# Performance work log

Measured on AMD Instinct MI355X. Metric: run time of the kernel, lower is better.

Reference implementation:

```python
import jax, jax.numpy as jnp
import numpy as np

B, S, D = 1, 2048, 2048
H, G, HD = 32, 8, 64
EPS = 1e-6
ROPE_BASE = 10000.0


def rms_norm(x, g):
    # torch RMSNorm computed in fp32 then cast back (PytorchRMSNorm wrapper)
    xf = x.astype(jnp.float32)
    y = xf * jax.lax.rsqrt(jnp.mean(xf * xf, axis=-1, keepdims=True) + EPS) * g.astype(jnp.float32)
    return y.astype(x.dtype)


def rotate_half(x):
    x1, x2 = jnp.split(x, 2, axis=-1)
    return jnp.concatenate([-x2, x1], axis=-1)


def apply_rope(x, cos, sin):
    # x: (b, h, s, hd); cos/sin: (s, hd)
    return x * cos[None, None] + rotate_half(x) * sin[None, None]


def setup_inputs() -> dict:
    key = jax.random.key(0)
    ks = jax.random.split(key, 8)
    x = jax.random.normal(ks[0], (B, S, D), dtype=jnp.float32)
    wq = jax.random.normal(ks[1], (H * HD, D), dtype=jnp.float32) * (D ** -0.5)
    wk = jax.random.normal(ks[2], (G * HD, D), dtype=jnp.float32) * (D ** -0.5)
    wv = jax.random.normal(ks[3], (G * HD, D), dtype=jnp.float32) * (D ** -0.5)
    wo = jax.random.normal(ks[4], (D, H * HD), dtype=jnp.float32) * (D ** -0.5)
    qg = jnp.ones((HD,), dtype=jnp.float32)
    kg = jnp.ones((HD,), dtype=jnp.float32)
    # RoPE tables (HF-style: duplicated half-dim frequencies)
    inv_freq = 1.0 / (ROPE_BASE ** (jnp.arange(0, HD, 2, dtype=jnp.float32) / HD))
    ang = jnp.arange(S, dtype=jnp.float32)[:, None] * inv_freq[None, :]  # (S, HD/2)
    emb = jnp.concatenate([ang, ang], axis=-1)  # (S, HD)
    cos = jnp.cos(emb)
    sin = jnp.sin(emb)
    # causal mask: True = future (upper-right triangle)
    mask = jnp.triu(jnp.ones((S, S), dtype=bool), k=1)
    return {"x": x, "mask": mask, "cos": cos, "sin": sin,
            "wq": wq, "wk": wk, "wv": wv, "wo": wo, "qg": qg, "kg": kg}


def reference(x, mask, cos, sin, wq, wk, wv, wo, qg, kg):
    b, s, _ = x.shape
    rep = H // G
    q = (x @ wq.T).reshape(b, s, H, HD).transpose(0, 2, 1, 3)   # (b,H,s,hd)
    k = (x @ wk.T).reshape(b, s, G, HD).transpose(0, 2, 1, 3)   # (b,G,s,hd)
    v = (x @ wv.T).reshape(b, s, G, HD).transpose(0, 2, 1, 3)
    q = rms_norm(q, qg)
    k = rms_norm(k, kg)
    q = apply_rope(q, cos[:s], sin[:s])
    k = apply_rope(k, cos[:s], sin[:s])
    k = jnp.repeat(k, rep, axis=1)  # (b,H,s,hd) GQA expansion
    v = jnp.repeat(v, rep, axis=1)
    scores = jnp.einsum('bhqd,bhkd->bhqk', q, k) * (HD ** -0.5)
    neg = jnp.finfo(scores.dtype).min / 2
    scores = jnp.where(mask[None, None, :s, :s], neg, scores)
    w = jax.nn.softmax(scores, axis=-1)
    ctx = jnp.einsum('bhqk,bhkd->bhqd', w, v)
    ctx = ctx.transpose(0, 2, 1, 3).reshape(b, s, H * HD)
    return ctx @ wo.T
```

## Files before the change

kernel.cpp:

```cpp
#include <hip/hip_runtime.h>
#include <stdint.h>

#define SEQ    2048
#define DMODEL 2048
#define NHEAD  32
#define NKV    8
#define HDIM   64
#define NQKV   3072

typedef __bf16 bf16x8 __attribute__((ext_vector_type(8)));
typedef float  f32x4  __attribute__((ext_vector_type(4)));

#define SCALE2 0.180336880f
#define THR2   12.0f

__device__ __forceinline__ ushort bf(float f){
  __bf16 h = (__bf16)f;
  return __builtin_bit_cast(unsigned short, h);
}
__device__ __forceinline__ float b2f(ushort v){
  union { uint32_t u; float f; } a; a.u = ((uint32_t)v) << 16; return a.f;
}
__device__ __forceinline__ float ex2(float x){
  return __builtin_amdgcn_exp2f(x);
}
__device__ __forceinline__ float fmax3(float a, float b, float c){
  float r;
  asm("v_max3_f32 %0, %1, %2, %3" : "=v"(r) : "v"(a), "v"(b), "v"(c));
  return r;
}

__device__ __forceinline__ void gl_lds16(const void* g, void* l){
  __builtin_amdgcn_global_load_lds(
      (const __attribute__((address_space(1))) uint32_t*)g,
      (__attribute__((address_space(3))) uint32_t*)l, 16, 0, 0);
}

__global__ __launch_bounds__(256) void k_cvt_all(const float* __restrict__ x,
                                                 const float* __restrict__ wq,
                                                 const float* __restrict__ wk,
                                                 const float* __restrict__ wv,
                                                 const float* __restrict__ wo,
                                                 ushort* __restrict__ xb,
                                                 ushort* __restrict__ wcat,
                                                 ushort* __restrict__ wob){
  int i = blockIdx.x * 256 + threadIdx.x;
  const float* src; ushort* dst; int s4; int d4;
  if (i < 1048576)      { src = x;  dst = xb;   s4 = i;           d4 = s4; }
  else if (i < 2097152) { src = wq; dst = wcat; s4 = i - 1048576; d4 = s4; }
  else if (i < 2359296) { src = wk; dst = wcat; s4 = i - 2097152; d4 = s4 + 1048576; }
  else if (i < 2621440) { src = wv; dst = wcat; s4 = i - 2359296; d4 = s4 + 1310720; }
  else                  { src = wo; dst = wob;  s4 = i - 2621440; d4 = s4; }
  float4 v = reinterpret_cast<const float4*>(src)[s4];
  ushort4 o;
  o.x = bf(v.x); o.y = bf(v.y); o.z = bf(v.z); o.w = bf(v.w);
  reinterpret_cast<ushort4*>(dst)[d4] = o;
}

__global__ __launch_bounds__(256) void k_gemm_bt(const ushort* __restrict__ A,
                                                 const ushort* __restrict__ B,
                                                 float* __restrict__ C,
                                                 int M, int N, int K){
  __shared__ ushort As[2][128*64];
  __shared__ ushort Bs[2][64*64];
  const int tid = threadIdx.x, lane = tid & 63, wid = tid >> 6;
  const int bm = blockIdx.y * 128, bn = blockIdx.x * 64;
  const int wr = wid >> 1, wc = wid & 1;
  const int l15 = lane & 15, u = lane >> 4;

  const int crow = lane >> 3;
  const int scol = ((lane & 7) ^ crow) * 8;
  const ushort* Abase = A + (size_t)(bm + wid*32 + crow) * K + scol;
  const ushort* Bbase = B + (size_t)(bn + wid*16 + crow) * K + scol;

  auto STAGE = [&](int buf, int k0){
#pragma unroll
    for (int c = 0; c < 4; c++)
      gl_lds16(Abase + k0 + (size_t)c*8*K, &As[buf][(wid*32 + c*8)*64]);
#pragma unroll
    for (int c = 0; c < 2; c++)
      gl_lds16(Bbase + k0 + (size_t)c*8*K, &Bs[buf][(wid*16 + c*8)*64]);
  };

  f32x4 acc[4][2] = {};
  const int NT = K >> 6;

  STAGE(0, 0);
  __syncthreads();

  for (int t = 0; t < NT; t++){
    const int cur = t & 1;
    if (t + 1 < NT) STAGE(cur ^ 1, (t + 1) << 6);

#pragma unroll
    for (int kc = 0; kc < 2; kc++){
      bf16x8 af[4], bfr[2];
#pragma unroll
      for (int m = 0; m < 4; m++){
        int row = wr*64 + m*16 + l15;
        af[m] = *reinterpret_cast<const bf16x8*>(&As[cur][row*64 + (((kc*4+u) ^ (row&7))*8)]);
      }
#pragma unroll
      for (int n = 0; n < 2; n++){
        int row = wc*32 + n*16 + l15;
        bfr[n] = *reinterpret_cast<const bf16x8*>(&Bs[cur][row*64 + (((kc*4+u) ^ (row&7))*8)]);
      }
      __builtin_amdgcn_s_setprio(1);
#pragma unroll
      for (int m = 0; m < 4; m++)
#pragma unroll
        for (int n = 0; n < 2; n++)
          acc[m][n] = __builtin_amdgcn_mfma_f32_16x16x32_bf16(af[m], bfr[n], acc[m][n], 0, 0, 0);
      __builtin_amdgcn_s_setprio(0);
    }

    __syncthreads();
  }

#pragma unroll
  for (int m = 0; m < 4; m++)
#pragma unroll
    for (int n = 0; n < 2; n++)
#pragma unroll
      for (int j = 0; j < 4; j++){
        int row = bm + wr*64 + m*16 + u*4 + j;
        int col = bn + wc*32 + n*16 + l15;
        C[(size_t)row * N + col] = acc[m][n][j];
      }
}

__global__ __launch_bounds__(256) void k_gemm_btc(const ushort* __restrict__ A,
                                                  const ushort* __restrict__ B,
                                                  ushort* __restrict__ C,
                                                  int M, int N, int K){
  __shared__ ushort As[2][128*64];
  __shared__ ushort Bs[2][96*64];
  const int tid = threadIdx.x, lane = tid & 63, wid = tid >> 6;
  const int bm = blockIdx.y * 128, bn = blockIdx.x * 96;
  const int wr = wid >> 1, wc = wid & 1;
  const int l15 = lane & 15, u = lane >> 4;

  const int crow = lane >> 3;
  const int scol = ((lane & 7) ^ crow) * 8;
  const ushort* Abase = A + (size_t)(bm + wid*32 + crow) * K + scol;
  const ushort* Bbase = B + (size_t)(bn + wid*24 + crow) * K + scol;

  auto STAGE = [&](int buf, int k0){
#pragma unroll
    for (int c = 0; c < 4; c++)
      gl_lds16(Abase + k0 + (size_t)c*8*K, &As[buf][(wid*32 + c*8)*64]);
#pragma unroll
    for (int c = 0; c < 3; c++)
      gl_lds16(Bbase + k0 + (size_t)c*8*K, &Bs[buf][(wid*24 + c*8)*64]);
  };

  f32x4 acc[4][3] = {};
  const int NT = K >> 6;

  STAGE(0, 0);
  __syncthreads();

  for (int t = 0; t < NT; t++){
    const int cur = t & 1;
    if (t + 1 < NT) STAGE(cur ^ 1, (t + 1) << 6);

#pragma unroll
    for (int kc = 0; kc < 2; kc++){
      bf16x8 af[4], bfr[3];
#pragma unroll
      for (int m = 0; m < 4; m++){
        int row = wr*64 + m*16 + l15;
        af[m] = *reinterpret_cast<const bf16x8*>(&As[cur][row*64 + (((kc*4+u) ^ (row&7))*8)]);
      }
#pragma unroll
      for (int n = 0; n < 3; n++){
        int row = wc*48 + n*16 + l15;
        bfr[n] = *reinterpret_cast<const bf16x8*>(&Bs[cur][row*64 + (((kc*4+u) ^ (row&7))*8)]);
      }
      __builtin_amdgcn_s_setprio(1);
#pragma unroll
      for (int m = 0; m < 4; m++)
#pragma unroll
        for (int n = 0; n < 3; n++)
          acc[m][n] = __builtin_amdgcn_mfma_f32_16x16x32_bf16(af[m], bfr[n], acc[m][n], 0, 0, 0);
      __builtin_amdgcn_s_setprio(0);
    }

    __syncthreads();
  }

#pragma unroll
  for (int m = 0; m < 4; m++)
#pragma unroll
    for (int n = 0; n < 3; n++)
#pragma unroll
      for (int j = 0; j < 4; j++){
        int row = bm + wr*64 + m*16 + u*4 + j;
        int col = bn + wc*48 + n*16 + l15;
        C[(size_t)row * N + col] = bf(acc[m][n][j]);
      }
}

__global__ __launch_bounds__(256) void k_normrope(const ushort* __restrict__ qkvc,
                                                  const float* __restrict__ cosp,
                                                  const float* __restrict__ sinp,
                                                  const float* __restrict__ qg,
                                                  const float* __restrict__ kg,
                                                  ushort* __restrict__ qb,
                                                  ushort* __restrict__ kb){
  const int s = blockIdx.x;
  const int tid = threadIdx.x, lane = tid & 63, wid = tid >> 6;
  const ushort* row = qkvc + (size_t)s * NQKV;
  const float cs = cosp[s*HDIM + lane];
  const float sn = sinp[s*HDIM + lane];

  for (int hidx = wid; hidx < 40; hidx += 4){
    const bool isq = hidx < 32;
    const int col = isq ? hidx*64 : 2048 + (hidx-32)*64;
    float x = b2f(row[col + lane]);
    float ss = x * x;
#pragma unroll
    for (int m = 1; m < 64; m <<= 1) ss += __shfl_xor(ss, m);
    float r = rsqrtf(ss * (1.0f/64.0f) + 1e-6f);
    float y = x * r * (isq ? qg : kg)[lane];
    float p = __shfl_xor(y, 32);
    float out = y * cs + (lane < 32 ? -p : p) * sn;
    if (isq) qb[(size_t)s*2048 + hidx*64 + lane] = bf(out * SCALE2);
    else     kb[(size_t)s*512 + (hidx-32)*64 + lane] = bf(out);
  }
}

__global__ __launch_bounds__(256) void k_vtrans(const ushort* __restrict__ qkvc,
                                                ushort* __restrict__ vtb){
  __shared__ ushort tile[64][68];
  const int g = blockIdx.x >> 5, st = blockIdx.x & 31;
  const int tid = threadIdx.x;
#pragma unroll
  for (int i = 0; i < 4; i++){
    int idx = i*256 + tid;
    int r = idx >> 4, c4 = idx & 15;
    ushort4 v = *reinterpret_cast<const ushort4*>(
        qkvc + (size_t)(st*64 + r)*NQKV + 2560 + g*64 + c4*4);
    tile[c4*4+0][r] = v.x;
    tile[c4*4+1][r] = v.y;
    tile[c4*4+2][r] = v.z;
    tile[c4*4+3][r] = v.w;
  }
  __syncthreads();
#pragma unroll
  for (int i = 0; i < 4; i++){
    int idx = i*256 + tid;
    int d = idx >> 4, s4 = idx & 15;
    int pos4 = (s4 >> 3)*32 + (s4 & 3)*8 + ((s4 >> 2) & 1)*4;
    ushort4 o = *reinterpret_cast<const ushort4*>(&tile[d][s4*4]);
    *reinterpret_cast<ushort4*>(vtb + (size_t)(g*64 + d)*SEQ + st*64 + pos4) = o;
  }
}

__global__ __launch_bounds__(256) void k_attn(const ushort* __restrict__ qbuf,
                                              const ushort* __restrict__ kbuf,
                                              const ushort* __restrict__ vtb,
                                              ushort* __restrict__ op,
                                              float2* __restrict__ ml){
  __shared__ ushort Kd[2][64*64];
  __shared__ ushort Vd[2][64*64];

  const int bx = blockIdx.x;
  const int qt   = 31 - (bx >> 6);
  const int part = (bx >> 5) & 1;
  const int h    = bx & 31;
  const int g = h >> 2;
  const int n  = qt + 1;
  const int h1 = (n + 1) >> 1;
  const int t0 = part ? h1 : 0;
  const int t1 = part ? n  : h1;
  const int tid = threadIdx.x, lane = tid & 63, wid = tid >> 6;
  const int l15 = lane & 15, u = lane >> 4;
  const int q0 = qt*64 + wid*16;

  bf16x8 qf[2];
#pragma unroll
  for (int kc = 0; kc < 2; kc++)
    qf[kc] = *reinterpret_cast<const bf16x8*>(
        qbuf + (size_t)(q0 + l15)*2048 + h*64 + kc*32 + u*8);

  f32x4 o[4] = {};
  float mrun = -1e30f;
  float lrun = 0.f;

  int koff[8], voff[8];
#pragma unroll
  for (int kb = 0; kb < 4; kb++)
#pragma unroll
    for (int kc = 0; kc < 2; kc++){
      int keyl = kb*16 + l15;
      koff[kb*2+kc] = (keyl*64 + (((kc*4+u) ^ (keyl&7))*8)) * 2;
    }
#pragma unroll
  for (int kc = 0; kc < 2; kc++)
#pragma unroll
    for (int d0 = 0; d0 < 4; d0++){
      int vrow = d0*16 + l15;
      voff[kc*4+d0] = (vrow*64 + (((kc*4+u) ^ (vrow&7))*8)) * 2;
    }

  const int srow = wid*16 + (lane >> 3);
  const int scol = ((lane & 7) ^ (lane >> 3)) * 8;
  const ushort* ksrc0 = kbuf + (size_t)srow*512 + g*64 + scol;
  const ushort* vsrc0 = vtb  + (size_t)(g*64 + srow)*SEQ + scol;

  auto STAGE = [&](int buf, int t){
    const ushort* ks = ksrc0 + (size_t)t*64*512;
    gl_lds16(ks,         &Kd[buf][wid*1024]);
    gl_lds16(ks + 8*512, &Kd[buf][wid*1024 + 512]);
    const ushort* vs = vsrc0 + t*64;
    gl_lds16(vs,          &Vd[buf][wid*1024]);
    gl_lds16(vs + 8*SEQ,  &Vd[buf][wid*1024 + 512]);
  };

  if (t0 < t1){
    STAGE(0, t0);
    __syncthreads();

    for (int t = t0; t < t1; t++){
      const int cur = (t - t0) & 1;
      if (t + 1 < t1) STAGE(cur ^ 1, t + 1);

      const char* KB = (const char*)Kd + cur*8192;
      const char* VB = (const char*)Vd + cur*8192;
      const bool full = (t*64 + 63) <= q0;

      f32x4 st[4];
#pragma unroll
      for (int kb = 0; kb < 4; kb++){
        const int key0 = t*64 + kb*16;
        if (key0 <= q0 + 15){
          bf16x8 kf0 = *reinterpret_cast<const bf16x8*>(KB + koff[kb*2]);
          bf16x8 kf1 = *reinterpret_cast<const bf16x8*>(KB + koff[kb*2+1]);
          f32x4 a = {};
          a = __builtin_amdgcn_mfma_f32_16x16x32_bf16(kf0, qf[0], a, 0, 0, 0);
          a = __builtin_amdgcn_mfma_f32_16x16x32_bf16(kf1, qf[1], a, 0, 0, 0);
          st[kb] = a;
        } else {
          st[kb] = (f32x4){-1e30f, -1e30f, -1e30f, -1e30f};
        }
      }
      if (!full){
        const int keyb = t*64 + u*4;
        const int qr = q0 + l15;
#pragma unroll
        for (int kb = 0; kb < 4; kb++)
#pragma unroll
          for (int j = 0; j < 4; j++)
            st[kb][j] = (keyb + kb*16 + j > qr) ? -1e30f : st[kb][j];
      }

      {
        float r0 = fmax3(st[0][0], st[0][1], st[0][2]);
        float r1 = fmax3(st[0][3], st[1][0], st[1][1]);
        float r2 = fmax3(st[1][2], st[1][3], st[2][0]);
        float r3 = fmax3(st[2][1], st[2][2], st[2][3]);
        float r4 = fmax3(st[3][0], st[3][1], st[3][2]);
        float m0 = fmax3(r0, r1, r2);
        float m1 = fmax3(r3, r4, st[3][3]);
        float tml = fmaxf(m0, m1);
        if (__any(tml > mrun + THR2)){
          float tm = fmaxf(tml, __shfl_xor(tml, 16));
          tm = fmaxf(tm, __shfl_xor(tm, 32));
          float mn = fmaxf(mrun, tm);
          float al = ex2(mrun - mn);
          mrun = mn;
          lrun *= al;
#pragma unroll
          for (int d0 = 0; d0 < 4; d0++)
#pragma unroll
            for (int j = 0; j < 4; j++) o[d0][j] *= al;
        }
        float ls[4];
#pragma unroll
        for (int kb = 0; kb < 4; kb++){
          float p0 = ex2(st[kb][0] - mrun);
          float p1 = ex2(st[kb][1] - mrun);
          float p2 = ex2(st[kb][2] - mrun);
          float p3 = ex2(st[kb][3] - mrun);
          st[kb][0] = p0; st[kb][1] = p1; st[kb][2] = p2; st[kb][3] = p3;
          ls[kb] = (p0 + p1) + (p2 + p3);
        }
        lrun += (ls[0] + ls[1]) + (ls[2] + ls[3]);
      }

      __builtin_amdgcn_s_setprio(1);
#pragma unroll
      for (int kc = 0; kc < 2; kc++){
        union { uint32_t w[4]; bf16x8 v; } pb;
        asm("v_cvt_pk_bf16_f32 %0, %1, %2" : "=v"(pb.w[0]) : "v"(st[2*kc  ][0]), "v"(st[2*kc  ][1]));
        asm("v_cvt_pk_bf16_f32 %0, %1, %2" : "=v"(pb.w[1]) : "v"(st[2*kc  ][2]), "v"(st[2*kc  ][3]));
        asm("v_cvt_pk_bf16_f32 %0, %1, %2" : "=v"(pb.w[2]) : "v"(st[2*kc+1][0]), "v"(st[2*kc+1][1]));
        asm("v_cvt_pk_bf16_f32 %0, %1, %2" : "=v"(pb.w[3]) : "v"(st[2*kc+1][2]), "v"(st[2*kc+1][3]));
#pragma unroll
        for (int d0 = 0; d0 < 4; d0++){
          bf16x8 vb8 = *reinterpret_cast<const bf16x8*>(VB + voff[kc*4+d0]);
          o[d0] = __builtin_amdgcn_mfma_f32_16x16x32_bf16(vb8, pb.v, o[d0], 0, 0, 0);
        }
      }
      __builtin_amdgcn_s_setprio(0);

      __syncthreads();
    }
  }

  {
    float lt = lrun + __shfl_xor(lrun, 16);
    lt += __shfl_xor(lt, 32);
    float inv = lt > 0.f ? 1.0f / lt : 0.f;
    const size_t ridx = (size_t)part*65536 + h*2048 + (q0 + l15);
#pragma unroll
    for (int d0 = 0; d0 < 4; d0++){
      ushort4 w;
      w.x = bf(o[d0][0] * inv); w.y = bf(o[d0][1] * inv);
      w.z = bf(o[d0][2] * inv); w.w = bf(o[d0][3] * inv);
      *reinterpret_cast<ushort4*>(&op[ridx*64 + d0*16 + u*4]) = w;
    }
    if (lane < 16) ml[ridx] = make_float2(mrun, lt);
  }
}

__global__ __launch_bounds__(256) void k_comb(const ushort* __restrict__ op,
                                              const float2* __restrict__ ml,
                                              ushort* __restrict__ ctx){
  const int tq = blockIdx.x*256 + threadIdx.x;
  const int q = tq & 3, row = (tq >> 2) & 2047, h = tq >> 13;
  const int idx = h*2048 + row;
  float2 a = ml[idx], b = ml[idx + 65536];
  float m = fmaxf(a.x, b.x);
  float w0 = ex2(a.x - m) * a.y;
  float w1 = ex2(b.x - m) * b.y;
  float inv = 1.0f / (w0 + w1);
  w0 *= inv; w1 *= inv;
  const ushort4* p0 = reinterpret_cast<const ushort4*>(op + (size_t)idx*64 + q*16);
  const ushort4* p1 = reinterpret_cast<const ushort4*>(op + ((size_t)idx + 65536)*64 + q*16);
  ushort* dst = ctx + (size_t)row*2048 + h*64 + q*16;
#pragma unroll
  for (int i = 0; i < 4; i++){
    ushort4 x0 = p0[i], x1 = p1[i];
    ushort4 w;
    w.x = bf(w0*b2f(x0.x) + w1*b2f(x1.x));
    w.y = bf(w0*b2f(x0.y) + w1*b2f(x1.y));
    w.z = bf(w0*b2f(x0.z) + w1*b2f(x1.z));
    w.w = bf(w0*b2f(x0.w) + w1*b2f(x1.w));
    reinterpret_cast<ushort4*>(dst)[i] = w;
  }
}

extern "C" void kernel_launch(void* const* d_in, const int* in_sizes, int n_in,
                              void* d_out, int out_size, void* d_ws, size_t ws_size,
                              hipStream_t stream){
  const float* x    = (const float*)d_in[0];
  const float* cosp = (const float*)d_in[2];
  const float* sinp = (const float*)d_in[3];
  const float* wq   = (const float*)d_in[4];
  const float* wk   = (const float*)d_in[5];
  const float* wv   = (const float*)d_in[6];
  const float* wo   = (const float*)d_in[7];
  const float* qg   = (const float*)d_in[8];
  const float* kg   = (const float*)d_in[9];
  float* out = (float*)d_out;

  char* ws = (char*)d_ws;
  ushort* xb   = (ushort*)(ws);
  ushort* wcat = (ushort*)(ws + 8388608);
  ushort* wob  = (ushort*)(ws + 20971520);
  ushort* qkvc = (ushort*)(ws + 29360128);
  ushort* qb   = (ushort*)(ws + 41943040);
  ushort* kb   = (ushort*)(ws + 50331648);
  ushort* vtb  = (ushort*)(ws + 52428800);
  ushort* ctxb = (ushort*)(ws + 54525952);
  ushort* op   = (ushort*)(ws);
  float2* ml   = (float2*)(ws + 16777216);

  k_cvt_all<<<14336, 256, 0, stream>>>(x, wq, wk, wv, wo, xb, wcat, wob);
  k_gemm_btc<<<dim3(32, 16), 256, 0, stream>>>(xb, wcat, qkvc, 2048, 3072, 2048);
  k_normrope<<<2048, 256, 0, stream>>>(qkvc, cosp, sinp, qg, kg, qb, kb);
  k_vtrans<<<256, 256, 0, stream>>>(qkvc, vtb);
  k_attn<<<2048, 256, 0, stream>>>(qb, kb, vtb, op, ml);
  k_comb<<<1024, 256, 0, stream>>>(op, ml, ctxb);
  k_gemm_bt<<<dim3(32, 16), 256, 0, stream>>>(ctxb, wob, out, 2048, 2048, 2048);
}
```

Measured before the change: 135.6 us.

## Process 128-row query tiles per block to reuse K/V fragments across two sub-tiles

Each wave now handles 32 query rows (two 16-row sub-tiles) instead of 16, so every K and V fragment read from LDS feeds two MFMAs. The grid is halved and the split-KV scheme is rewritten so each 128-row tile splits its causal key range evenly into two parts. Query tiles are paired (j and 15-j) to balance the causal work across blocks. This doubles accumulator and score registers per thread, and the kernel now asks for 4 blocks per CU via launch bounds, which risks register spills.

```diff
diff --git a/kernel.cpp b/kernel.cpp
--- a/kernel.cpp
+++ b/kernel.cpp
@@ -257,36 +257,37 @@
   }
 }
 
-__global__ __launch_bounds__(256) void k_attn(const ushort* __restrict__ qbuf,
-                                              const ushort* __restrict__ kbuf,
-                                              const ushort* __restrict__ vtb,
-                                              ushort* __restrict__ op,
-                                              float2* __restrict__ ml){
+__global__ __launch_bounds__(256, 4) void k_attn(const ushort* __restrict__ qbuf,
+                                                 const ushort* __restrict__ kbuf,
+                                                 const ushort* __restrict__ vtb,
+                                                 ushort* __restrict__ op,
+                                                 float2* __restrict__ ml){
   __shared__ ushort Kd[2][64*64];
   __shared__ ushort Vd[2][64*64];
 
   const int bx = blockIdx.x;
-  const int qt   = 31 - (bx >> 6);
-  const int part = (bx >> 5) & 1;
-  const int h    = bx & 31;
+  const int c = bx & 255, slot = bx >> 8;
+  const int h = c >> 3, j = c & 7;
+  const int qt   = (slot & 1) ? j : 15 - j;
+  const int part = slot >> 1;
   const int g = h >> 2;
-  const int n  = qt + 1;
-  const int h1 = (n + 1) >> 1;
-  const int t0 = part ? h1 : 0;
-  const int t1 = part ? n  : h1;
+  const int t0 = part ? (qt + 1)   : 0;
+  const int t1 = part ? (2*qt + 2) : (qt + 1);
   const int tid = threadIdx.x, lane = tid & 63, wid = tid >> 6;
   const int l15 = lane & 15, u = lane >> 4;
-  const int q0 = qt*64 + wid*16;
-
-  bf16x8 qf[2];
-#pragma unroll
-  for (int kc = 0; kc < 2; kc++)
-    qf[kc] = *reinterpret_cast<const bf16x8*>(
-        qbuf + (size_t)(q0 + l15)*2048 + h*64 + kc*32 + u*8);
-
-  f32x4 o[4] = {};
-  float mrun = -1e30f;
-  float lrun = 0.f;
+  const int q0 = qt*128 + wid*32;
+
+  bf16x8 qf[2][2];
+#pragma unroll
+  for (int hh = 0; hh < 2; hh++)
+#pragma unroll
+    for (int kc = 0; kc < 2; kc++)
+      qf[hh][kc] = *reinterpret_cast<const bf16x8*>(
+          qbuf + (size_t)(q0 + hh*16 + l15)*2048 + h*64 + kc*32 + u*8);
+
+  f32x4 o[2][4] = {};
+  float mrun[2] = {-1e30f, -1e30f};
+  float lrun[2] = {0.f, 0.f};
 
   int koff[8], voff[8];
 #pragma unroll
@@ -318,110 +319,120 @@
     gl_lds16(vs + 8*SEQ,  &Vd[buf][wid*1024 + 512]);
   };
 
-  if (t0 < t1){
-    STAGE(0, t0);
+  STAGE(0, t0);
+  __syncthreads();
+
+  for (int t = t0; t < t1; t++){
+    const int cur = (t - t0) & 1;
+    if (t + 1 < t1) STAGE(cur ^ 1, t + 1);
+
+    const char* KB = (const char*)Kd + cur*8192;
+    const char* VB = (const char*)Vd + cur*8192;
+
+    f32x4 st[2][4];
+#pragma unroll
+    for (int kb = 0; kb < 4; kb++){
+      const int key0 = t*64 + kb*16;
+      bf16x8 kf0 = *reinterpret_cast<const bf16x8*>(KB + koff[kb*2]);
+      bf16x8 kf1 = *reinterpret_cast<const bf16x8*>(KB + koff[kb*2+1]);
+#pragma unroll
+      for (int hh = 0; hh < 2; hh++){
+        if (key0 <= q0 + hh*16 + 15){
+          f32x4 a = {};
+          a = __builtin_amdgcn_mfma_f32_16x16x32_bf16(kf0, qf[hh][0], a, 0, 0, 0);
+          a = __builtin_amdgcn_mfma_f32_16x16x32_bf16(kf1, qf[hh][1], a, 0, 0, 0);
+          st[hh][kb] = a;
+        } else {
+          st[hh][kb] = (f32x4){-1e30f, -1e30f, -1e30f, -1e30f};
+        }
+      }
+    }
+#pragma unroll
+    for (int hh = 0; hh < 2; hh++){
+      if (!((t*64 + 63) <= q0 + hh*16)){
+        const int keyb = t*64 + u*4;
+        const int qr = q0 + hh*16 + l15;
+#pragma unroll
+        for (int kb = 0; kb < 4; kb++)
+#pragma unroll
+          for (int jj = 0; jj < 4; jj++)
+            st[hh][kb][jj] = (keyb + kb*16 + jj > qr) ? -1e30f : st[hh][kb][jj];
+      }
+    }
+
+#pragma unroll
+    for (int hh = 0; hh < 2; hh++){
+      float r0 = fmax3(st[hh][0][0], st[hh][0][1], st[hh][0][2]);
+      float r1 = fmax3(st[hh][0][3], st[hh][1][0], st[hh][1][1]);
+      float r2 = fmax3(st[hh][1][2], st[hh][1][3], st[hh][2][0]);
+      float r3 = fmax3(st[hh][2][1], st[hh][2][2], st[hh][2][3]);
+      float r4 = fmax3(st[hh][3][0], st[hh][3][1], st[hh][3][2]);
+      float m0 = fmax3(r0, r1, r2);
+      float m1 = fmax3(r3, r4, st[hh][3][3]);
+      float tml = fmaxf(m0, m1);
+      if (__any(tml > mrun[hh] + THR2)){
+        float tm = fmaxf(tml, __shfl_xor(tml, 16));
+        tm = fmaxf(tm, __shfl_xor(tm, 32));
+        float mn = fmaxf(mrun[hh], tm);
+        float al = ex2(mrun[hh] - mn);
+        mrun[hh] = mn;
+        lrun[hh] *= al;
+#pragma unroll
+        for (int d0 = 0; d0 < 4; d0++)
+#pragma unroll
+          for (int jj = 0; jj < 4; jj++) o[hh][d0][jj] *= al;
+      }
+      float ls[4];
+#pragma unroll
+      for (int kb = 0; kb < 4; kb++){
+        float p0 = ex2(st[hh][kb][0] - mrun[hh]);
+        float p1 = ex2(st[hh][kb][1] - mrun[hh]);
+        float p2 = ex2(st[hh][kb][2] - mrun[hh]);
+        float p3 = ex2(st[hh][kb][3] - mrun[hh]);
+        st[hh][kb][0] = p0; st[hh][kb][1] = p1;
+        st[hh][kb][2] = p2; st[hh][kb][3] = p3;
+        ls[kb] = (p0 + p1) + (p2 + p3);
+      }
+      lrun[hh] += (ls[0] + ls[1]) + (ls[2] + ls[3]);
+    }
+
+    __builtin_amdgcn_s_setprio(1);
+#pragma unroll
+    for (int kc = 0; kc < 2; kc++){
+      union { uint32_t w[4]; bf16x8 v; } pb[2];
+#pragma unroll
+      for (int hh = 0; hh < 2; hh++){
+        asm("v_cvt_pk_bf16_f32 %0, %1, %2" : "=v"(pb[hh].w[0]) : "v"(st[hh][2*kc  ][0]), "v"(st[hh][2*kc  ][1]));
+        asm("v_cvt_pk_bf16_f32 %0, %1, %2" : "=v"(pb[hh].w[1]) : "v"(st[hh][2*kc  ][2]), "v"(st[hh][2*kc  ][3]));
+        asm("v_cvt_pk_bf16_f32 %0, %1, %2" : "=v"(pb[hh].w[2]) : "v"(st[hh][2*kc+1][0]), "v"(st[hh][2*kc+1][1]));
+        asm("v_cvt_pk_bf16_f32 %0, %1, %2" : "=v"(pb[hh].w[3]) : "v"(st[hh][2*kc+1][2]), "v"(st[hh][2*kc+1][3]));
+      }
+#pragma unroll
+      for (int d0 = 0; d0 < 4; d0++){
+        bf16x8 vb8 = *reinterpret_cast<const bf16x8*>(VB + voff[kc*4+d0]);
+        o[0][d0] = __builtin_amdgcn_mfma_f32_16x16x32_bf16(vb8, pb[0].v, o[0][d0], 0, 0, 0);
+        o[1][d0] = __builtin_amdgcn_mfma_f32_16x16x32_bf16(vb8, pb[1].v, o[1][d0], 0, 0, 0);
+      }
+    }
+    __builtin_amdgcn_s_setprio(0);
+
     __syncthreads();
-
-    for (int t = t0; t < t1; t++){
-      const int cur = (t - t0) & 1;
-      if (t + 1 < t1) STAGE(cur ^ 1, t + 1);
-
-      const char* KB = (const char*)Kd + cur*8192;
-      const char* VB = (const char*)Vd + cur*8192;
-      const bool full = (t*64 + 63) <= q0;
-
-      f32x4 st[4];
-#pragma unroll
-      for (int kb = 0; kb < 4; kb++){
-        const int key0 = t*64 + kb*16;
-        if (key0 <= q0 + 15){
-          bf16x8 kf0 = *reinterpret_cast<const bf16x8*>(KB + koff[kb*2]);
-          bf16x8 kf1 = *reinterpret_cast<const bf16x8*>(KB + koff[kb*2+1]);
-          f32x4 a = {};
-          a = __builtin_amdgcn_mfma_f32_16x16x32_bf16(kf0, qf[0], a, 0, 0, 0);
-          a = __builtin_amdgcn_mfma_f32_16x16x32_bf16(kf1, qf[1], a, 0, 0, 0);
-          st[kb] = a;
-        } else {
-          st[kb] = (f32x4){-1e30f, -1e30f, -1e30f, -1e30f};
-        }
-      }
-      if (!full){
-        const int keyb = t*64 + u*4;
-        const int qr = q0 + l15;
-#pragma unroll
-        for (int kb = 0; kb < 4; kb++)
-#pragma unroll
-          for (int j = 0; j < 4; j++)
-            st[kb][j] = (keyb + kb*16 + j > qr) ? -1e30f : st[kb][j];
-      }
-
-      {
-        float r0 = fmax3(st[0][0], st[0][1], st[0][2]);
-        float r1 = fmax3(st[0][3], st[1][0], st[1][1]);
-        float r2 = fmax3(st[1][2], st[1][3], st[2][0]);
-        float r3 = fmax3(st[2][1], st[2][2], st[2][3]);
-        float r4 = fmax3(st[3][0], st[3][1], st[3][2]);
-        float m0 = fmax3(r0, r1, r2);
-        float m1 = fmax3(r3, r4, st[3][3]);
-        float tml = fmaxf(m0, m1);
-        if (__any(tml > mrun + THR2)){
-          float tm = fmaxf(tml, __shfl_xor(tml, 16));
-          tm = fmaxf(tm, __shfl_xor(tm, 32));
-          float mn = fmaxf(mrun, tm);
-          float al = ex2(mrun - mn);
-          mrun = mn;
-          lrun *= al;
-#pragma unroll
-          for (int d0 = 0; d0 < 4; d0++)
-#pragma unroll
-            for (int j = 0; j < 4; j++) o[d0][j] *= al;
-        }
-        float ls[4];
-#pragma unroll
-        for (int kb = 0; kb < 4; kb++){
-          float p0 = ex2(st[kb][0] - mrun);
-          float p1 = ex2(st[kb][1] - mrun);
-          float p2 = ex2(st[kb][2] - mrun);
-          float p3 = ex2(st[kb][3] - mrun);
-          st[kb][0] = p0; st[kb][1] = p1; st[kb][2] = p2; st[kb][3] = p3;
-          ls[kb] = (p0 + p1) + (p2 + p3);
-        }
-        lrun += (ls[0] + ls[1]) + (ls[2] + ls[3]);
-      }
-
-      __builtin_amdgcn_s_setprio(1);
-#pragma unroll
-      for (int kc = 0; kc < 2; kc++){
-        union { uint32_t w[4]; bf16x8 v; } pb;
-        asm("v_cvt_pk_bf16_f32 %0, %1, %2" : "=v"(pb.w[0]) : "v"(st[2*kc  ][0]), "v"(st[2*kc  ][1]));
-        asm("v_cvt_pk_bf16_f32 %0, %1, %2" : "=v"(pb.w[1]) : "v"(st[2*kc  ][2]), "v"(st[2*kc  ][3]));
-        asm("v_cvt_pk_bf16_f32 %0, %1, %2" : "=v"(pb.w[2]) : "v"(st[2*kc+1][0]), "v"(st[2*kc+1][1]));
-        asm("v_cvt_pk_bf16_f32 %0, %1, %2" : "=v"(pb.w[3]) : "v"(st[2*kc+1][2]), "v"(st[2*kc+1][3]));
-#pragma unroll
-        for (int d0 = 0; d0 < 4; d0++){
-          bf16x8 vb8 = *reinterpret_cast<const bf16x8*>(VB + voff[kc*4+d0]);
-          o[d0] = __builtin_amdgcn_mfma_f32_16x16x32_bf16(vb8, pb.v, o[d0], 0, 0, 0);
-        }
-      }
-      __builtin_amdgcn_s_setprio(0);
-
-      __syncthreads();
-    }
-  }
-
-  {
-    float lt = lrun + __shfl_xor(lrun, 16);
+  }
+
+#pragma unroll
+  for (int hh = 0; hh < 2; hh++){
+    float lt = lrun[hh] + __shfl_xor(lrun[hh], 16);
     lt += __shfl_xor(lt, 32);
     float inv = lt > 0.f ? 1.0f / lt : 0.f;
-    const size_t ridx = (size_t)part*65536 + h*2048 + (q0 + l15);
+    const size_t ridx = (size_t)part*65536 + h*2048 + (q0 + hh*16 + l15);
 #pragma unroll
     for (int d0 = 0; d0 < 4; d0++){
       ushort4 w;
-      w.x = bf(o[d0][0] * inv); w.y = bf(o[d0][1] * inv);
-      w.z = bf(o[d0][2] * inv); w.w = bf(o[d0][3] * inv);
+      w.x = bf(o[hh][d0][0] * inv); w.y = bf(o[hh][d0][1] * inv);
+      w.z = bf(o[hh][d0][2] * inv); w.w = bf(o[hh][d0][3] * inv);
       *reinterpret_cast<ushort4*>(&op[ridx*64 + d0*16 + u*4]) = w;
     }
-    if (lane < 16) ml[ridx] = make_float2(mrun, lt);
+    if (lane < 16) ml[ridx] = make_float2(mrun[hh], lt);
   }
 }
 
@@ -482,7 +493,7 @@
   k_gemm_btc<<<dim3(32, 16), 256, 0, stream>>>(xb, wcat, qkvc, 2048, 3072, 2048);
   k_normrope<<<2048, 256, 0, stream>>>(qkvc, cosp, sinp, qg, kg, qb, kb);
   k_vtrans<<<256, 256, 0, stream>>>(qkvc, vtb);
-  k_attn<<<2048, 256, 0, stream>>>(qb, kb, vtb, op, ml);
+  k_attn<<<1024, 256, 0, stream>>>(qb, kb, vtb, op, ml);
   k_comb<<<1024, 256, 0, stream>>>(op, ml, ctxb);
   k_gemm_bt<<<dim3(32, 16), 256, 0, stream>>>(ctxb, wob, out, 2048, 2048, 2048);
 }
```

Measured after the change: 130.6 us. 1.04x faster.
